# Performance work log

Hardware: AMD Instinct MI355X
Metric: run time of the kernel (lower is better)

## Reference

```python
import jax, jax.numpy as jnp
import numpy as np

B, T1, T2, NFEAT, H = 8, 512, 1500, 1024, 16
DK = NFEAT // H


def setup_inputs() -> dict:
    key = jax.random.key(0)
    ks = jax.random.split(key, 8)
    s = 0.02
    return {
        "x": jax.random.normal(ks[0], (B, T1, NFEAT), dtype=jnp.float32),
        "memory": jax.random.normal(ks[1], (B, T2, NFEAT), dtype=jnp.float32),
        "memory_mask": jnp.ones((B, 1, T2), dtype=jnp.int32),
        "Wq": jax.random.normal(ks[2], (NFEAT, NFEAT), dtype=jnp.float32) * s,
        "bq": jnp.zeros((NFEAT,), dtype=jnp.float32),
        "Wkv": jax.random.normal(ks[3], (NFEAT, 2 * NFEAT), dtype=jnp.float32) * s,
        "bkv": jnp.zeros((2 * NFEAT,), dtype=jnp.float32),
        "Wout": jax.random.normal(ks[4], (NFEAT, NFEAT), dtype=jnp.float32) * s,
        "bout": jnp.zeros((NFEAT,), dtype=jnp.float32),
    }


def reference(x, memory, memory_mask, Wq, bq, Wkv, bkv, Wout, bout):
    b, t1, _ = x.shape
    t2 = memory.shape[1]
    # projections (W stored as (in, out))
    q = x @ Wq + bq                                   # (b, t1, n_feat)
    kv = memory @ Wkv + bkv                           # (b, t2, 2*n_feat)
    k, v = jnp.split(kv, 2, axis=-1)
    q_h = q.reshape(b, t1, H, DK).transpose(0, 2, 1, 3)   # (b,h,t1,dk)
    k_h = k.reshape(b, t2, H, DK).transpose(0, 2, 1, 3)   # (b,h,t2,dk)
    v_h = v.reshape(b, t2, H, DK).transpose(0, 2, 1, 3)   # (b,h,t2,dk)
    q_h = q_h * (DK ** -0.5)
    scores = jnp.einsum("bhqd,bhkd->bhqk", q_h, k_h)      # (b,h,t1,t2)
    mask0 = (memory_mask[:, None, :, :] == 0)             # (b,1,1 or t1,t2)
    scores = jnp.where(mask0, -jnp.inf, scores)
    attn = jax.nn.softmax(scores, axis=-1)
    attn = jnp.where(mask0, 0.0, attn)
    ctx = jnp.einsum("bhqk,bhkd->bhqd", attn, v_h)        # (b,h,t1,dk)
    ctx = ctx.transpose(0, 2, 1, 3).reshape(b, t1, H * DK)
    return ctx @ Wout + bout
```

## Files before the change

### kernel.cpp

```cpp
#include <hip/hip_runtime.h>
#include <cstdint>
#include <cstddef>

typedef __attribute__((ext_vector_type(8))) short short8;
typedef __attribute__((ext_vector_type(4))) float f32x4;

typedef __attribute__((address_space(3))) unsigned int lds_u32;
typedef const __attribute__((address_space(1))) unsigned int glb_u32;

__device__ __forceinline__ void gl_lds16(const void* g, void* l) {
  __builtin_amdgcn_global_load_lds((glb_u32*)g, (lds_u32*)l, 16, 0, 0);
}

__device__ __forceinline__ unsigned short bf16_rne(float f) {
  unsigned int u = __float_as_uint(f);
  u += 0x7FFFu + ((u >> 16) & 1u);
  return (unsigned short)(u >> 16);
}

__device__ __forceinline__ void cvt_body(const float* __restrict__ in,
                                         unsigned short* __restrict__ out,
                                         int i, int n8) {
  if (i >= n8) return;
  float4 a = reinterpret_cast<const float4*>(in)[2 * i];
  float4 b = reinterpret_cast<const float4*>(in)[2 * i + 1];
  short8 v;
  v[0] = (short)bf16_rne(a.x); v[1] = (short)bf16_rne(a.y);
  v[2] = (short)bf16_rne(a.z); v[3] = (short)bf16_rne(a.w);
  v[4] = (short)bf16_rne(b.x); v[5] = (short)bf16_rne(b.y);
  v[6] = (short)bf16_rne(b.z); v[7] = (short)bf16_rne(b.w);
  reinterpret_cast<short8*>(out)[i] = v;
}

__global__ void __launch_bounds__(256) k_prep(const float* __restrict__ x,
                                              const float* __restrict__ mem,
                                              const float* __restrict__ Wq,
                                              const float* __restrict__ Wkv,
                                              const float* __restrict__ Wout,
                                              unsigned short* __restrict__ xb,
                                              unsigned short* __restrict__ mb,
                                              unsigned short* __restrict__ wqT,
                                              unsigned short* __restrict__ wkvT,
                                              unsigned short* __restrict__ woutT,
                                              unsigned short* __restrict__ pk,
                                              unsigned short* __restrict__ pv) {
  __shared__ float t[64][65];
  const int bid = blockIdx.x, tid = threadIdx.x;
  if (bid < 2048) {
    cvt_body(x, xb, bid * 256 + tid, 524288);
  } else if (bid < 8048) {
    cvt_body(mem, mb, (bid - 2048) * 256 + tid, 1536000);
  } else if (bid < 9072) {
    const float* W; unsigned short* WT; int R = 1024, C; int bid2, bx, by;
    if (bid < 8304)      { W = Wq;   WT = wqT;   C = 1024; bid2 = bid - 8048; bx = bid2 & 15; by = bid2 >> 4; }
    else if (bid < 8816) { W = Wkv;  WT = wkvT;  C = 2048; bid2 = bid - 8304; bx = bid2 & 31; by = bid2 >> 5; }
    else                 { W = Wout; WT = woutT; C = 1024; bid2 = bid - 8816; bx = bid2 & 15; by = bid2 >> 4; }
    const int c0 = bx * 64, r0 = by * 64;
    const int lr = tid >> 6, lc = tid & 63;
#pragma unroll
    for (int i = 0; i < 16; ++i)
      t[i * 4 + lr][lc] = W[(size_t)(r0 + i * 4 + lr) * C + c0 + lc];
    __syncthreads();
#pragma unroll
    for (int i = 0; i < 16; ++i) {
      int ro = i * 4 + lr;
      WT[(size_t)(c0 + ro) * R + r0 + lc] = bf16_rne(t[lc][ro]);
    }
  } else {
    int i = (bid - 9072) * 256 + tid;
    if (i >= 128 * 36 * 64) return;
    int head = i / (36 * 64);
    int rem = i - head * (36 * 64);
    int t2 = rem / 64 + 1500;
    int dk = rem & 63;
    size_t ik = ((size_t)(head * 24 + 23) * 8 + (dk >> 3)) * 512 + (t2 & 63) * 8 + (dk & 7);
    size_t iv = ((size_t)(head * 24 + 23) * 8 + ((t2 >> 3) & 7)) * 512 + dk * 8 + (t2 & 7);
    pk[ik] = 0;
    pv[iv] = 0;
  }
}

template <int MODE>
__global__ void __launch_bounds__(256) k_gemm(const unsigned short* __restrict__ A,
                                              const unsigned short* __restrict__ BT,
                                              const float* __restrict__ bias,
                                              void* __restrict__ out1,
                                              void* __restrict__ out2,
                                              int M, int K) {
  __shared__ unsigned short As[2][128 * 64];
  __shared__ unsigned short Bs[2][128 * 64];
  const int tid = threadIdx.x;
  const int lane = tid & 63;
  const int wid = tid >> 6;
  const int grp = lane >> 4, lm = lane & 15;

  constexpr int NBY = (MODE == 1) ? 16 : 8;
  constexpr int NWG = (MODE == 1) ? 94 * 16 : 32 * 8;
  constexpr int CPX = NWG / 8;
  const int bid = blockIdx.x;
  const int logical = (bid & 7) * CPX + (bid >> 3);
  const int m0 = (logical / NBY) * 128, n0 = (logical % NBY) * 128;

  const int wm = (wid >> 1) * 64, wn = (wid & 1) * 64;
  const int srow = tid >> 3;
  const int sx = ((tid & 7) * 16) ^ ((srow & 7) << 4);

  const int nkt = K >> 6;
#pragma unroll
  for (int c = 0; c < 4; ++c) {
    int row = c * 32 + srow;
    int ra = m0 + row; if (ra > M - 1) ra = M - 1;
    gl_lds16(A + (size_t)ra * K + (sx >> 1), &As[0][c * 2048 + tid * 8]);
    gl_lds16(BT + (size_t)(n0 + row) * K + (sx >> 1), &Bs[0][c * 2048 + tid * 8]);
  }
  __syncthreads();

  f32x4 acc[4][4] = {};
  int cur = 0;
  for (int kt = 0; kt < nkt; ++kt) {
    if (kt + 1 < nkt) {
#pragma unroll
      for (int c = 0; c < 4; ++c) {
        int row = c * 32 + srow;
        int ra = m0 + row; if (ra > M - 1) ra = M - 1;
        gl_lds16(A + (size_t)ra * K + (kt + 1) * 64 + (sx >> 1),
                 &As[cur ^ 1][c * 2048 + tid * 8]);
        gl_lds16(BT + (size_t)(n0 + row) * K + (kt + 1) * 64 + (sx >> 1),
                 &Bs[cur ^ 1][c * 2048 + tid * 8]);
      }
    }

    const unsigned short* Ab = &As[cur][0];
    const unsigned short* Bb = &Bs[cur][0];
    short8 af[4][2], bfr[4][2];
#pragma unroll
    for (int m = 0; m < 4; ++m)
#pragma unroll
      for (int ks = 0; ks < 2; ++ks) {
        int row = wm + m * 16 + lm;
        int off = (ks * 64 + grp * 16) ^ ((row & 7) << 4);
        af[m][ks] = *reinterpret_cast<const short8*>(&Ab[row * 64 + (off >> 1)]);
      }
#pragma unroll
    for (int n = 0; n < 4; ++n)
#pragma unroll
      for (int ks = 0; ks < 2; ++ks) {
        int row = wn + n * 16 + lm;
        int off = (ks * 64 + grp * 16) ^ ((row & 7) << 4);
        bfr[n][ks] = *reinterpret_cast<const short8*>(&Bb[row * 64 + (off >> 1)]);
      }
#pragma unroll
    for (int m = 0; m < 4; ++m)
#pragma unroll
      for (int n = 0; n < 4; ++n)
#pragma unroll
        for (int ks = 0; ks < 2; ++ks)
          acc[m][n] = __builtin_amdgcn_mfma_f32_16x16x32_bf16(af[m][ks], bfr[n][ks],
                                                              acc[m][n], 0, 0, 0);
    __syncthreads();
    cur ^= 1;
  }

#pragma unroll
  for (int m = 0; m < 4; ++m) {
    int rbase = m0 + wm + m * 16 + grp * 4;
#pragma unroll
    for (int n = 0; n < 4; ++n) {
      int cg = n0 + wn + n * 16 + lm;
      float bs = bias[cg];
#pragma unroll
      for (int r = 0; r < 4; ++r) {
        int row = rbase + r;
        float v = acc[m][n][r] + bs;
        if (MODE == 0) {
          v *= 0.180336884f;
          int b = row >> 9, t1 = row & 511, h = cg >> 6, dk = cg & 63;
          ((unsigned short*)out1)[(((size_t)b * 16 + h) * 512 + t1) * 64 + dk] = bf16_rne(v);
        } else if (MODE == 1) {
          if (row < M) {
            int b = row / 1500, t2 = row - b * 1500;
            if (cg < 1024) {
              int h = cg >> 6, dk = cg & 63;
              int head = b * 16 + h;
              size_t idx = ((size_t)(head * 24 + (t2 >> 6)) * 8 + (dk >> 3)) * 512 +
                           (t2 & 63) * 8 + (dk & 7);
              ((unsigned short*)out1)[idx] = bf16_rne(v);
            } else {
              int h = (cg - 1024) >> 6, dk = (cg - 1024) & 63;
              int head = b * 16 + h;
              size_t idx = ((size_t)(head * 24 + (t2 >> 6)) * 8 + ((t2 >> 3) & 7)) * 512 +
                           dk * 8 + (t2 & 7);
              ((unsigned short*)out2)[idx] = bf16_rne(v);
            }
          }
        } else {
          ((float*)out1)[(size_t)row * 1024 + cg] = v;
        }
      }
    }
  }
}

__global__ void __launch_bounds__(256) k_attn(const unsigned short* __restrict__ Q,
                                              const unsigned short* __restrict__ PK,
                                              const unsigned short* __restrict__ PV,
                                              const int* __restrict__ mask,
                                              float* __restrict__ po,
                                              float* __restrict__ dn) {
  __shared__ unsigned short Ps[4][16 * 64];
  const int tid = threadIdx.x, lane = tid & 63, wid = tid >> 6;
  const int grp = lane >> 4, lm = lane & 15;
  const int bid = blockIdx.x;
  const int logical = (bid & 7) * 256 + (bid >> 3);
  const int head = logical >> 4, qt = (logical >> 1) & 7, half = logical & 1;
  const int b = head >> 4, h = head & 15;
  const int kt0 = half * 12;

  const unsigned short* qbase = Q + ((size_t)head * 512 + qt * 64) * 64;
  const unsigned short* kf = PK + (size_t)head * 98304 + grp * 512 + lm * 8;
  const unsigned short* vf = PV + (size_t)head * 98304 + grp * 512 + lm * 8;
  const int* mrow = mask + b * 1500;

  short8 aq[2];
#pragma unroll
  for (int ks = 0; ks < 2; ++ks)
    aq[ks] = *reinterpret_cast<const short8*>(qbase + (wid * 16 + lm) * 64 + ks * 32 + grp * 8);

  unsigned long long mlo = 0ull;
#pragma unroll
  for (int i = 0; i < 48; ++i) {
    int col = (kt0 + (i >> 2)) * 64 + (i & 3) * 16 + lm;
    unsigned int ok = (col < 1500) ? (mrow[col] != 0 ? 1u : 0u) : 0u;
    mlo |= (unsigned long long)ok << i;
  }

  f32x4 O[4] = {};
  f32x4 O4 = {0.f, 0.f, 0.f, 0.f};
  const short8 onesb = {(short)0x3F80, (short)0x3F80, (short)0x3F80, (short)0x3F80,
                        (short)0x3F80, (short)0x3F80, (short)0x3F80, (short)0x3F80};

  short8 bk[4][2];
#pragma unroll
  for (int n = 0; n < 4; ++n)
#pragma unroll
    for (int ks = 0; ks < 2; ++ks)
      bk[n][ks] = *reinterpret_cast<const short8*>(kf + (size_t)kt0 * 4096 + ks * 2048 + n * 128);

  for (int kt = kt0; kt < kt0 + 12; ++kt) {
    short8 bv[4][2];
#pragma unroll
    for (int n2 = 0; n2 < 4; ++n2)
#pragma unroll
      for (int ks = 0; ks < 2; ++ks)
        bv[n2][ks] = *reinterpret_cast<const short8*>(vf + (size_t)kt * 4096 + ks * 2048 + n2 * 128);

    f32x4 s[4];
#pragma unroll
    for (int n = 0; n < 4; ++n) {
      s[n] = f32x4{0.f, 0.f, 0.f, 0.f};
#pragma unroll
      for (int ks = 0; ks < 2; ++ks)
        s[n] = __builtin_amdgcn_mfma_f32_16x16x32_bf16(aq[ks], bk[n][ks], s[n], 0, 0, 0);
    }

    if (kt < kt0 + 11) {
#pragma unroll
      for (int n = 0; n < 4; ++n)
#pragma unroll
        for (int ks = 0; ks < 2; ++ks)
          bk[n][ks] = *reinterpret_cast<const short8*>(
              kf + (size_t)(kt + 1) * 4096 + ks * 2048 + n * 128);
    }

    unsigned int nib = (unsigned int)mlo & 15u;
    mlo >>= 4;
    float mb4[4];
#pragma unroll
    for (int n = 0; n < 4; ++n) mb4[n] = (nib >> n) & 1u ? -8.0f : -3.0e38f;
#pragma unroll
    for (int n = 0; n < 4; ++n)
#pragma unroll
      for (int r = 0; r < 4; ++r) s[n][r] = exp2f(s[n][r] + mb4[n]);

#pragma unroll
    for (int n = 0; n < 4; ++n)
#pragma unroll
      for (int r = 0; r < 4; ++r) {
        int prow = grp * 4 + r;
        int pb = (n * 16 + lm) * 2;
        Ps[wid][prow * 64 + ((pb ^ ((prow & 7) << 4)) >> 1)] = bf16_rne(s[n][r]);
      }
    short8 pa[2];
#pragma unroll
    for (int ks = 0; ks < 2; ++ks) {
      int off = (ks * 64 + grp * 16) ^ ((lm & 7) << 4);
      pa[ks] = *reinterpret_cast<const short8*>(&Ps[wid][lm * 64 + (off >> 1)]);
    }

#pragma unroll
    for (int n2 = 0; n2 < 4; ++n2)
#pragma unroll
      for (int ks = 0; ks < 2; ++ks)
        O[n2] = __builtin_amdgcn_mfma_f32_16x16x32_bf16(pa[ks], bv[n2][ks], O[n2], 0, 0, 0);
#pragma unroll
    for (int ks = 0; ks < 2; ++ks)
      O4 = __builtin_amdgcn_mfma_f32_16x16x32_bf16(pa[ks], onesb, O4, 0, 0, 0);
  }

  float* orow = po + (size_t)half * 4194304 +
                ((size_t)(b * 512 + qt * 64 + wid * 16 + grp * 4)) * 1024 + h * 64;
#pragma unroll
  for (int r = 0; r < 4; ++r)
#pragma unroll
    for (int n2 = 0; n2 < 4; ++n2)
      orow[r * 1024 + n2 * 16 + lm] = O[n2][r];
  if (lm == 0) {
    int t1g = b * 512 + qt * 64 + wid * 16 + grp * 4;
#pragma unroll
    for (int r = 0; r < 4; ++r)
      dn[half * 65536 + (t1g + r) * 16 + h] = O4[r];
  }
}

__global__ void __launch_bounds__(256) k_comb(const float* __restrict__ po,
                                              const float* __restrict__ dn,
                                              unsigned short* __restrict__ ctx) {
  int idx = blockIdx.x * 256 + threadIdx.x;
  if (idx >= 524288) return;
  int row = idx >> 7, c8 = idx & 127;
  int col0 = c8 * 8, h = c8 >> 3;
  float d = dn[row * 16 + h] + dn[65536 + row * 16 + h];
  float inv = 1.0f / d;
  const float4* p0 = reinterpret_cast<const float4*>(po + (size_t)row * 1024 + col0);
  const float4* p1 = reinterpret_cast<const float4*>(po + 4194304 + (size_t)row * 1024 + col0);
  float4 a0 = p0[0], a1 = p0[1], b0 = p1[0], b1 = p1[1];
  short8 v;
  v[0] = (short)bf16_rne((a0.x + b0.x) * inv);
  v[1] = (short)bf16_rne((a0.y + b0.y) * inv);
  v[2] = (short)bf16_rne((a0.z + b0.z) * inv);
  v[3] = (short)bf16_rne((a0.w + b0.w) * inv);
  v[4] = (short)bf16_rne((a1.x + b1.x) * inv);
  v[5] = (short)bf16_rne((a1.y + b1.y) * inv);
  v[6] = (short)bf16_rne((a1.z + b1.z) * inv);
  v[7] = (short)bf16_rne((a1.w + b1.w) * inv);
  reinterpret_cast<short8*>(ctx)[idx] = v;
}

extern "C" void kernel_launch(void* const* d_in, const int* in_sizes, int n_in,
                              void* d_out, int out_size, void* d_ws, size_t ws_size,
                              hipStream_t stream) {
  const float* x = (const float*)d_in[0];
  const float* mem = (const float*)d_in[1];
  const int* mask = (const int*)d_in[2];
  const float* Wq = (const float*)d_in[3];
  const float* bq = (const float*)d_in[4];
  const float* Wkv = (const float*)d_in[5];
  const float* bkv = (const float*)d_in[6];
  const float* Wout = (const float*)d_in[7];
  const float* bout = (const float*)d_in[8];

  uint8_t* w = (uint8_t*)d_ws;
  unsigned short* xb    = (unsigned short*)(w);
  unsigned short* mb    = (unsigned short*)(w + 8388608);
  unsigned short* wqT   = (unsigned short*)(w + 32964608);
  unsigned short* wkvT  = (unsigned short*)(w + 35061760);
  unsigned short* woutT = (unsigned short*)(w + 39256064);
  unsigned short* qb    = (unsigned short*)(w + 41353216);
  unsigned short* kb    = (unsigned short*)(w + 49741824);
  unsigned short* vtb   = (unsigned short*)(w + 74907648);
  unsigned short* ctx   = (unsigned short*)(w + 100073472);
  float* po             = (float*)(w);
  float* dn             = (float*)(w + 33554432);

  k_prep<<<10224, 256, 0, stream>>>(x, mem, Wq, Wkv, Wout, xb, mb, wqT, wkvT, woutT, kb, vtb);
  k_gemm<0><<<256, 256, 0, stream>>>(xb, wqT, bq, qb, nullptr, 4096, 1024);
  k_gemm<1><<<1504, 256, 0, stream>>>(mb, wkvT, bkv, kb, vtb, 12000, 1024);
  k_attn<<<2048, 256, 0, stream>>>(qb, kb, vtb, mask, po, dn);
  k_comb<<<2048, 256, 0, stream>>>(po, dn, ctx);
  k_gemm<2><<<256, 256, 0, stream>>>(ctx, woutT, bout, d_out, nullptr, 4096, 1024);
}
```

Baseline: 219.1 us.

## Fuse Q/KV GEMMs, fold split-combine into output GEMM, drop GEMM double buffering

```diff
diff --git a/kernel.cpp b/kernel.cpp
--- a/kernel.cpp
+++ b/kernel.cpp
@@ -16,6 +16,13 @@
   unsigned int u = __float_as_uint(f);
   u += 0x7FFFu + ((u >> 16) & 1u);
   return (unsigned short)(u >> 16);
+}
+
+__device__ __forceinline__ short8 pack8(const float* v) {
+  short8 r;
+#pragma unroll
+  for (int e = 0; e < 8; ++e) r[e] = (short)bf16_rne(v[e]);
+  return r;
 }
 
 __device__ __forceinline__ void cvt_body(const float* __restrict__ in,
@@ -24,12 +31,8 @@
   if (i >= n8) return;
   float4 a = reinterpret_cast<const float4*>(in)[2 * i];
   float4 b = reinterpret_cast<const float4*>(in)[2 * i + 1];
-  short8 v;
-  v[0] = (short)bf16_rne(a.x); v[1] = (short)bf16_rne(a.y);
-  v[2] = (short)bf16_rne(a.z); v[3] = (short)bf16_rne(a.w);
-  v[4] = (short)bf16_rne(b.x); v[5] = (short)bf16_rne(b.y);
-  v[6] = (short)bf16_rne(b.z); v[7] = (short)bf16_rne(b.w);
-  reinterpret_cast<short8*>(out)[i] = v;
+  float v[8] = {a.x, a.y, a.z, a.w, b.x, b.y, b.z, b.w};
+  reinterpret_cast<short8*>(out)[i] = pack8(v);
 }
 
 __global__ void __launch_bounds__(256) k_prep(const float* __restrict__ x,
@@ -41,7 +44,7 @@
                                               unsigned short* __restrict__ mb,
                                               unsigned short* __restrict__ wqT,
                                               unsigned short* __restrict__ wkvT,
-                                              unsigned short* __restrict__ woutT,
+                                              unsigned short* __restrict__ wop,
                                               unsigned short* __restrict__ pk,
                                               unsigned short* __restrict__ pv) {
   __shared__ float t[64][65];
@@ -50,11 +53,10 @@
     cvt_body(x, xb, bid * 256 + tid, 524288);
   } else if (bid < 8048) {
     cvt_body(mem, mb, (bid - 2048) * 256 + tid, 1536000);
-  } else if (bid < 9072) {
-    const float* W; unsigned short* WT; int R = 1024, C; int bid2, bx, by;
-    if (bid < 8304)      { W = Wq;   WT = wqT;   C = 1024; bid2 = bid - 8048; bx = bid2 & 15; by = bid2 >> 4; }
-    else if (bid < 8816) { W = Wkv;  WT = wkvT;  C = 2048; bid2 = bid - 8304; bx = bid2 & 31; by = bid2 >> 5; }
-    else                 { W = Wout; WT = woutT; C = 1024; bid2 = bid - 8816; bx = bid2 & 15; by = bid2 >> 4; }
+  } else if (bid < 8816) {
+    const float* W; unsigned short* WT; int C, bid2, bx, by;
+    if (bid < 8304) { W = Wq;  WT = wqT;  C = 1024; bid2 = bid - 8048; bx = bid2 & 15; by = bid2 >> 4; }
+    else            { W = Wkv; WT = wkvT; C = 2048; bid2 = bid - 8304; bx = bid2 & 31; by = bid2 >> 5; }
     const int c0 = bx * 64, r0 = by * 64;
     const int lr = tid >> 6, lc = tid & 63;
 #pragma unroll
@@ -64,10 +66,22 @@
 #pragma unroll
     for (int i = 0; i < 16; ++i) {
       int ro = i * 4 + lr;
-      WT[(size_t)(c0 + ro) * R + r0 + lc] = bf16_rne(t[lc][ro]);
-    }
+      WT[(size_t)(c0 + ro) * 1024 + r0 + lc] = bf16_rne(t[lc][ro]);
+    }
+  } else if (bid < 9328) {
+    int w0 = (bid - 8816) * 256 + tid;
+    int rowN = w0 & 127; int tt = w0 >> 7;
+    int grp = tt & 3; tt >>= 2;
+    int ks = tt & 1; tt >>= 1;
+    int kt = tt & 15; int nblk = tt >> 4;
+    int n = nblk * 128 + rowN;
+    int k0 = kt * 64 + ks * 32 + grp * 8;
+    float v[8];
+#pragma unroll
+    for (int e = 0; e < 8; ++e) v[e] = Wout[(size_t)(k0 + e) * 1024 + n];
+    *reinterpret_cast<short8*>(wop + (size_t)w0 * 8) = pack8(v);
   } else {
-    int i = (bid - 9072) * 256 + tid;
+    int i = (bid - 9328) * 256 + tid;
     if (i >= 128 * 36 * 64) return;
     int head = i / (36 * 64);
     int rem = i - head * (36 * 64);
@@ -81,57 +95,40 @@
 }
 
 template <int MODE>
-__global__ void __launch_bounds__(256) k_gemm(const unsigned short* __restrict__ A,
-                                              const unsigned short* __restrict__ BT,
-                                              const float* __restrict__ bias,
-                                              void* __restrict__ out1,
-                                              void* __restrict__ out2,
-                                              int M, int K) {
-  __shared__ unsigned short As[2][128 * 64];
-  __shared__ unsigned short Bs[2][128 * 64];
+__device__ __forceinline__ void gemm_body(unsigned short* As, unsigned short* Bs,
+                                          const unsigned short* __restrict__ A,
+                                          const unsigned short* __restrict__ BT,
+                                          const float* __restrict__ bias,
+                                          void* __restrict__ out1,
+                                          void* __restrict__ out2,
+                                          int M, int bid) {
   const int tid = threadIdx.x;
   const int lane = tid & 63;
   const int wid = tid >> 6;
   const int grp = lane >> 4, lm = lane & 15;
-
+  constexpr int K = 1024;
   constexpr int NBY = (MODE == 1) ? 16 : 8;
-  constexpr int NWG = (MODE == 1) ? 94 * 16 : 32 * 8;
+  constexpr int NWG = (MODE == 1) ? 1504 : 256;
   constexpr int CPX = NWG / 8;
-  const int bid = blockIdx.x;
   const int logical = (bid & 7) * CPX + (bid >> 3);
   const int m0 = (logical / NBY) * 128, n0 = (logical % NBY) * 128;
-
   const int wm = (wid >> 1) * 64, wn = (wid & 1) * 64;
   const int srow = tid >> 3;
   const int sx = ((tid & 7) * 16) ^ ((srow & 7) << 4);
 
+  f32x4 acc[4][4] = {};
   const int nkt = K >> 6;
-#pragma unroll
-  for (int c = 0; c < 4; ++c) {
-    int row = c * 32 + srow;
-    int ra = m0 + row; if (ra > M - 1) ra = M - 1;
-    gl_lds16(A + (size_t)ra * K + (sx >> 1), &As[0][c * 2048 + tid * 8]);
-    gl_lds16(BT + (size_t)(n0 + row) * K + (sx >> 1), &Bs[0][c * 2048 + tid * 8]);
-  }
-  __syncthreads();
-
-  f32x4 acc[4][4] = {};
-  int cur = 0;
   for (int kt = 0; kt < nkt; ++kt) {
-    if (kt + 1 < nkt) {
-#pragma unroll
-      for (int c = 0; c < 4; ++c) {
-        int row = c * 32 + srow;
-        int ra = m0 + row; if (ra > M - 1) ra = M - 1;
-        gl_lds16(A + (size_t)ra * K + (kt + 1) * 64 + (sx >> 1),
-                 &As[cur ^ 1][c * 2048 + tid * 8]);
-        gl_lds16(BT + (size_t)(n0 + row) * K + (kt + 1) * 64 + (sx >> 1),
-                 &Bs[cur ^ 1][c * 2048 + tid * 8]);
-      }
-    }
-
-    const unsigned short* Ab = &As[cur][0];
-    const unsigned short* Bb = &Bs[cur][0];
+    __syncthreads();
+#pragma unroll
+    for (int c = 0; c < 4; ++c) {
+      int row = c * 32 + srow;
+      int ra = m0 + row; if (ra > M - 1) ra = M - 1;
+      gl_lds16(A + (size_t)ra * K + kt * 64 + (sx >> 1), As + c * 2048 + tid * 8);
+      gl_lds16(BT + (size_t)(n0 + row) * K + kt * 64 + (sx >> 1), Bs + c * 2048 + tid * 8);
+    }
+    __syncthreads();
+
     short8 af[4][2], bfr[4][2];
 #pragma unroll
     for (int m = 0; m < 4; ++m)
@@ -139,7 +136,7 @@
       for (int ks = 0; ks < 2; ++ks) {
         int row = wm + m * 16 + lm;
         int off = (ks * 64 + grp * 16) ^ ((row & 7) << 4);
-        af[m][ks] = *reinterpret_cast<const short8*>(&Ab[row * 64 + (off >> 1)]);
+        af[m][ks] = *reinterpret_cast<const short8*>(&As[row * 64 + (off >> 1)]);
       }
 #pragma unroll
     for (int n = 0; n < 4; ++n)
@@ -147,7 +144,7 @@
       for (int ks = 0; ks < 2; ++ks) {
         int row = wn + n * 16 + lm;
         int off = (ks * 64 + grp * 16) ^ ((row & 7) << 4);
-        bfr[n][ks] = *reinterpret_cast<const short8*>(&Bb[row * 64 + (off >> 1)]);
+        bfr[n][ks] = *reinterpret_cast<const short8*>(&Bs[row * 64 + (off >> 1)]);
       }
 #pragma unroll
     for (int m = 0; m < 4; ++m)
@@ -157,8 +154,6 @@
         for (int ks = 0; ks < 2; ++ks)
           acc[m][n] = __builtin_amdgcn_mfma_f32_16x16x32_bf16(af[m][ks], bfr[n][ks],
                                                               acc[m][n], 0, 0, 0);
-    __syncthreads();
-    cur ^= 1;
   }
 
 #pragma unroll
@@ -176,7 +171,7 @@
           v *= 0.180336884f;
           int b = row >> 9, t1 = row & 511, h = cg >> 6, dk = cg & 63;
           ((unsigned short*)out1)[(((size_t)b * 16 + h) * 512 + t1) * 64 + dk] = bf16_rne(v);
-        } else if (MODE == 1) {
+        } else {
           if (row < M) {
             int b = row / 1500, t2 = row - b * 1500;
             if (cg < 1024) {
@@ -193,10 +188,111 @@
               ((unsigned short*)out2)[idx] = bf16_rne(v);
             }
           }
-        } else {
-          ((float*)out1)[(size_t)row * 1024 + cg] = v;
         }
       }
+    }
+  }
+}
+
+__global__ void __launch_bounds__(256) k_gemm01(const unsigned short* __restrict__ xb,
+                                                const unsigned short* __restrict__ wqT,
+                                                const float* __restrict__ bq,
+                                                unsigned short* __restrict__ qb,
+                                                const unsigned short* __restrict__ mb,
+                                                const unsigned short* __restrict__ wkvT,
+                                                const float* __restrict__ bkv,
+                                                unsigned short* __restrict__ kb,
+                                                unsigned short* __restrict__ vtb) {
+  __shared__ unsigned short As[128 * 64];
+  __shared__ unsigned short Bs[128 * 64];
+  if (blockIdx.x < 1504)
+    gemm_body<1>(As, Bs, mb, wkvT, bkv, kb, vtb, 12000, blockIdx.x);
+  else
+    gemm_body<0>(As, Bs, xb, wqT, bq, qb, nullptr, 4096, blockIdx.x - 1504);
+}
+
+__global__ void __launch_bounds__(256) k_gemm2(const unsigned short* __restrict__ Bp,
+                                               const float* __restrict__ bias,
+                                               float* __restrict__ out1,
+                                               const float* __restrict__ po,
+                                               const float* __restrict__ dn) {
+  const int tid = threadIdx.x, lane = tid & 63, wid = tid >> 6;
+  const int grp = lane >> 4, lm = lane & 15;
+  constexpr int NKT = 16;
+  const int bid = blockIdx.x;
+  const int logical = (bid & 7) * 32 + (bid >> 3);
+  const int mblk = logical >> 3, nblk = logical & 7;
+  const int m0 = mblk * 128, n0 = nblk * 128;
+  const int wm = (wid >> 1) * 64, wn = (wid & 1) * 64;
+
+  const unsigned short* bb = Bp + (size_t)nblk * 131072 + grp * 1024 + (wn + lm) * 8;
+
+  f32x4 acc[4][4] = {};
+  short8 aA[4][2], bA[4][2], aB[4][2], bB[4][2];
+
+#define LOADB_(dst, kt)                                                          \
+  {                                                                              \
+    _Pragma("unroll") for (int n = 0; n < 4; ++n)                                \
+        _Pragma("unroll") for (int ks = 0; ks < 2; ++ks)                         \
+            dst[n][ks] = *reinterpret_cast<const short8*>(                       \
+                bb + ((kt) * 2 + ks) * 4096 + n * 128);                          \
+  }
+#define LOADA_(dst, kt)                                                          \
+  {                                                                              \
+    _Pragma("unroll") for (int m = 0; m < 4; ++m) {                              \
+      int row = m0 + wm + m * 16 + lm;                                           \
+      float inv = 1.0f / (dn[row * 16 + (kt)] + dn[65536 + row * 16 + (kt)]);    \
+      _Pragma("unroll") for (int ks = 0; ks < 2; ++ks) {                         \
+        const float* p0 = po + (size_t)row * 1024 + (kt) * 64 + ks * 32 + grp * 8; \
+        const float* p1 = p0 + 4194304;                                          \
+        float4 x0 = *reinterpret_cast<const float4*>(p0);                        \
+        float4 x1 = *reinterpret_cast<const float4*>(p0 + 4);                    \
+        float4 y0 = *reinterpret_cast<const float4*>(p1);                        \
+        float4 y1 = *reinterpret_cast<const float4*>(p1 + 4);                    \
+        float v[8] = {(x0.x + y0.x) * inv, (x0.y + y0.y) * inv,                  \
+                      (x0.z + y0.z) * inv, (x0.w + y0.w) * inv,                  \
+                      (x1.x + y1.x) * inv, (x1.y + y1.y) * inv,                  \
+                      (x1.z + y1.z) * inv, (x1.w + y1.w) * inv};                 \
+        dst[m][ks] = pack8(v);                                                   \
+      }                                                                          \
+    }                                                                            \
+  }
+#define MFMA_(a, b)                                                              \
+  {                                                                              \
+    _Pragma("unroll") for (int m = 0; m < 4; ++m)                                \
+        _Pragma("unroll") for (int n = 0; n < 4; ++n)                            \
+            _Pragma("unroll") for (int ks = 0; ks < 2; ++ks)                     \
+                acc[m][n] = __builtin_amdgcn_mfma_f32_16x16x32_bf16(             \
+                    a[m][ks], b[n][ks], acc[m][n], 0, 0, 0);                     \
+  }
+
+  LOADA_(aA, 0);
+  LOADB_(bA, 0);
+  for (int kt2 = 0; kt2 < NKT / 2; ++kt2) {
+    const int ktb = 2 * kt2 + 1;
+    LOADA_(aB, ktb);
+    LOADB_(bB, ktb);
+    MFMA_(aA, bA);
+    if (ktb + 1 < NKT) {
+      LOADA_(aA, ktb + 1);
+      LOADB_(bA, ktb + 1);
+    }
+    MFMA_(aB, bB);
+  }
+#undef LOADA_
+#undef LOADB_
+#undef MFMA_
+
+#pragma unroll
+  for (int m = 0; m < 4; ++m) {
+    int rbase = m0 + wm + m * 16 + grp * 4;
+#pragma unroll
+    for (int n = 0; n < 4; ++n) {
+      int cg = n0 + wn + n * 16 + lm;
+      float bs = bias[cg];
+#pragma unroll
+      for (int r = 0; r < 4; ++r)
+        out1[(size_t)(rbase + r) * 1024 + cg] = acc[m][n][r] + bs;
     }
   }
 }
@@ -322,30 +418,6 @@
   }
 }
 
-__global__ void __launch_bounds__(256) k_comb(const float* __restrict__ po,
-                                              const float* __restrict__ dn,
-                                              unsigned short* __restrict__ ctx) {
-  int idx = blockIdx.x * 256 + threadIdx.x;
-  if (idx >= 524288) return;
-  int row = idx >> 7, c8 = idx & 127;
-  int col0 = c8 * 8, h = c8 >> 3;
-  float d = dn[row * 16 + h] + dn[65536 + row * 16 + h];
-  float inv = 1.0f / d;
-  const float4* p0 = reinterpret_cast<const float4*>(po + (size_t)row * 1024 + col0);
-  const float4* p1 = reinterpret_cast<const float4*>(po + 4194304 + (size_t)row * 1024 + col0);
-  float4 a0 = p0[0], a1 = p0[1], b0 = p1[0], b1 = p1[1];
-  short8 v;
-  v[0] = (short)bf16_rne((a0.x + b0.x) * inv);
-  v[1] = (short)bf16_rne((a0.y + b0.y) * inv);
-  v[2] = (short)bf16_rne((a0.z + b0.z) * inv);
-  v[3] = (short)bf16_rne((a0.w + b0.w) * inv);
-  v[4] = (short)bf16_rne((a1.x + b1.x) * inv);
-  v[5] = (short)bf16_rne((a1.y + b1.y) * inv);
-  v[6] = (short)bf16_rne((a1.z + b1.z) * inv);
-  v[7] = (short)bf16_rne((a1.w + b1.w) * inv);
-  reinterpret_cast<short8*>(ctx)[idx] = v;
-}
-
 extern "C" void kernel_launch(void* const* d_in, const int* in_sizes, int n_in,
                               void* d_out, int out_size, void* d_ws, size_t ws_size,
                               hipStream_t stream) {
@@ -360,22 +432,19 @@
   const float* bout = (const float*)d_in[8];
 
   uint8_t* w = (uint8_t*)d_ws;
-  unsigned short* xb    = (unsigned short*)(w);
-  unsigned short* mb    = (unsigned short*)(w + 8388608);
-  unsigned short* wqT   = (unsigned short*)(w + 32964608);
-  unsigned short* wkvT  = (unsigned short*)(w + 35061760);
-  unsigned short* woutT = (unsigned short*)(w + 39256064);
-  unsigned short* qb    = (unsigned short*)(w + 41353216);
-  unsigned short* kb    = (unsigned short*)(w + 49741824);
-  unsigned short* vtb   = (unsigned short*)(w + 74907648);
-  unsigned short* ctx   = (unsigned short*)(w + 100073472);
-  float* po             = (float*)(w);
-  float* dn             = (float*)(w + 33554432);
-
-  k_prep<<<10224, 256, 0, stream>>>(x, mem, Wq, Wkv, Wout, xb, mb, wqT, wkvT, woutT, kb, vtb);
-  k_gemm<0><<<256, 256, 0, stream>>>(xb, wqT, bq, qb, nullptr, 4096, 1024);
-  k_gemm<1><<<1504, 256, 0, stream>>>(mb, wkvT, bkv, kb, vtb, 12000, 1024);
+  unsigned short* xb   = (unsigned short*)(w);
+  unsigned short* mb   = (unsigned short*)(w + 8388608);
+  unsigned short* wqT  = (unsigned short*)(w + 32964608);
+  unsigned short* wkvT = (unsigned short*)(w + 35061760);
+  unsigned short* wop  = (unsigned short*)(w + 39256064);
+  unsigned short* qb   = (unsigned short*)(w + 41353216);
+  unsigned short* kb   = (unsigned short*)(w + 49741824);
+  unsigned short* vtb  = (unsigned short*)(w + 74907648);
+  float* po            = (float*)(w);
+  float* dn            = (float*)(w + 33554432);
+
+  k_prep<<<10480, 256, 0, stream>>>(x, mem, Wq, Wkv, Wout, xb, mb, wqT, wkvT, wop, kb, vtb);
+  k_gemm01<<<1760, 256, 0, stream>>>(xb, wqT, bq, qb, mb, wkvT, bkv, kb, vtb);
   k_attn<<<2048, 256, 0, stream>>>(qb, kb, vtb, mask, po, dn);
-  k_comb<<<2048, 256, 0, stream>>>(po, dn, ctx);
-  k_gemm<2><<<256, 256, 0, stream>>>(ctx, woutT, bout, d_out, nullptr, 4096, 1024);
-}
+  k_gemm2<<<256, 256, 0, stream>>>(wop, bout, (float*)d_out, po, dn);
+}
```

New measurement: 262.1 us. 1.2x slower.
